# Kernel tuning notes

Measured on AMD Instinct MI355X. Metric: run time of the kernel, lower is better.

Reference implementation:

```python
import jax, jax.numpy as jnp
import numpy as np

D_MODEL = 512
N_HEADS = 8
D_KV = 64
EPS = 1e-6
ROPE_THETA = 10000.0


def _rms_norm(x, w):
    # T5-style RMSNorm: no mean subtraction, no bias, variance in fp32.
    var = jnp.mean(x.astype(jnp.float32) ** 2, axis=-1, keepdims=True)
    return (x * jax.lax.rsqrt(var + EPS)).astype(x.dtype) * w


def _rope_cos_sin(pos, dk):
    # pos: [B, T] int -> cos/sin: [B, 1, T, dk]
    inv_freq = 1.0 / (ROPE_THETA ** (jnp.arange(0, dk, 2, dtype=jnp.float32) / dk))
    ang = pos.astype(jnp.float32)[:, :, None] * inv_freq[None, None, :]  # [B,T,dk/2]
    ang = jnp.concatenate([ang, ang], axis=-1)                            # [B,T,dk]
    return jnp.cos(ang)[:, None], jnp.sin(ang)[:, None]


def _rotate_half(x):
    h = x.shape[-1] // 2
    return jnp.concatenate([-x[..., h:], x[..., :h]], axis=-1)


def _mha(x, mask, wq, wk, wv, wo, pos=None):
    # x: [B, T, D]; mask: [B, H, T, T] additive
    B, T, _ = x.shape
    def proj(w):
        return (x @ w).reshape(B, T, N_HEADS, D_KV).transpose(0, 2, 1, 3)  # [B,H,T,dk]
    q, k, v = proj(wq), proj(wk), proj(wv)
    if pos is not None:
        cos, sin = _rope_cos_sin(pos, D_KV)
        cos, sin = cos.astype(x.dtype), sin.astype(x.dtype)
        q = q * cos + _rotate_half(q) * sin
        k = k * cos + _rotate_half(k) * sin
    scale = 1.0 / np.sqrt(D_KV)
    scores = jnp.einsum('bhqd,bhkd->bhqk', q, k) * scale + mask
    attn = jax.nn.softmax(scores.astype(jnp.float32), axis=-1).astype(scores.dtype)
    out = jnp.einsum('bhqk,bhkd->bhqd', attn, v)
    out = out.transpose(0, 2, 1, 3).reshape(B, T, N_HEADS * D_KV)
    return out @ wo


def setup_inputs() -> dict:
    key = jax.random.key(0)
    ks = jax.random.split(key, 12)
    B, T = 8, 1024
    s = 1.0 / np.sqrt(D_MODEL)
    inp = {
        'h': jax.random.normal(ks[0], (B, T, D_MODEL), dtype=jnp.float32),
        'pos': jnp.broadcast_to(jnp.arange(T, dtype=jnp.int64 if jax.config.jax_enable_x64 else jnp.int32)[None, :], (B, T)),
        't_mask': jnp.zeros((B, N_HEADS, T, T), dtype=jnp.float32),
        'g_mask': jnp.zeros((T, N_HEADS, B, B), dtype=jnp.float32),
        'ln_t_w': jnp.ones((D_MODEL,), dtype=jnp.float32),
        'ln_g_w': jnp.ones((D_MODEL,), dtype=jnp.float32),
    }
    names = ['wq_t', 'wk_t', 'wv_t', 'wo_t', 'wq_g', 'wk_g', 'wv_g', 'wo_g']
    for i, n in enumerate(names):
        inp[n] = jax.random.normal(ks[i + 1], (D_MODEL, D_MODEL), dtype=jnp.float32) * s
    return inp


def reference(h, pos, t_mask, g_mask, ln_t_w, ln_g_w,
              wq_t, wk_t, wv_t, wo_t, wq_g, wk_g, wv_g, wo_g):
    # --- time attention (over T axis, with RoPE) ---
    normed = _rms_norm(h, ln_t_w)
    attn_t = _mha(normed, t_mask, wq_t, wk_t, wv_t, wo_t, pos=pos)
    h = h + attn_t  # dropout p=0 (eval)
    # --- group attention (over B axis, no RoPE) ---
    h = h.transpose(1, 0, 2)  # [T, B, D]
    normed = _rms_norm(h, ln_g_w)
    attn_g = _mha(normed, g_mask, wq_g, wk_g, wv_g, wo_g, pos=None)
    h = h + attn_g
    return h.transpose(1, 0, 2)  # back to [B, T, D]
```

## Files before the change

### kernel.cpp

```cpp
#include <hip/hip_runtime.h>
#include <hip/hip_bf16.h>
#include <math.h>


typedef __bf16 bf16x8 __attribute__((ext_vector_type(8)));
typedef __bf16 bf16x4 __attribute__((ext_vector_type(4)));
typedef float  f32x4  __attribute__((ext_vector_type(4)));

#define LN1E4_OVER_32 0.2878231366242558f

__device__ __forceinline__ void gld16(const void* g, void* l) {
    __builtin_amdgcn_global_load_lds((const __attribute__((address_space(1))) void*)g,
                                     (__attribute__((address_space(3))) void*)l,
                                     16, 0, 0);
}

__global__ __launch_bounds__(256) void transpose_w(
    const float* w0, const float* w1, const float* w2, const float* w3,
    const float* w4, const float* w5, const float* w6, const float* w7,
    __bf16* qkvT_t, __bf16* oT_t, __bf16* qkvT_g, __bf16* oT_g)
{
    int mat = blockIdx.z;
    const float* src; __bf16* dst; int rowOff;
    switch (mat) {
        case 0: src=w0; dst=qkvT_t; rowOff=0;    break;
        case 1: src=w1; dst=qkvT_t; rowOff=512;  break;
        case 2: src=w2; dst=qkvT_t; rowOff=1024; break;
        case 3: src=w3; dst=oT_t;   rowOff=0;    break;
        case 4: src=w4; dst=qkvT_g; rowOff=0;    break;
        case 5: src=w5; dst=qkvT_g; rowOff=512;  break;
        case 6: src=w6; dst=qkvT_g; rowOff=1024; break;
        default: src=w7; dst=oT_g;  rowOff=0;    break;
    }
    __shared__ float tile[32][33];
    int n0 = blockIdx.x * 32, k0 = blockIdx.y * 32;
    int tt = threadIdx.x;
    int kr = tt >> 3, nc = (tt & 7) * 4;
    float4 v = *(const float4*)(src + (size_t)(k0 + kr) * 512 + n0 + nc);
    tile[kr][nc+0] = v.x; tile[kr][nc+1] = v.y; tile[kr][nc+2] = v.z; tile[kr][nc+3] = v.w;
    __syncthreads();
    int nr = tt >> 3, kc = (tt & 7) * 4;
    bf16x4 o;
    o[0] = (__bf16)tile[kc+0][nr]; o[1] = (__bf16)tile[kc+1][nr];
    o[2] = (__bf16)tile[kc+2][nr]; o[3] = (__bf16)tile[kc+3][nr];
    *(bf16x4*)(dst + (size_t)(rowOff + n0 + nr) * 512 + k0 + kc) = o;
}

__global__ __launch_bounds__(256) void rmsnorm_k(
    const float* __restrict__ x, const float* __restrict__ w,
    __bf16* __restrict__ y, int remap)
{
    int row = blockIdx.x * 4 + (threadIdx.x >> 6);
    int l = threadIdx.x & 63;
    const float* xr = x + (size_t)row * 512 + l * 8;
    float4 a = *(const float4*)xr;
    float4 b = *(const float4*)(xr + 4);
    float ss = a.x*a.x + a.y*a.y + a.z*a.z + a.w*a.w
             + b.x*b.x + b.y*b.y + b.z*b.z + b.w*b.w;
    for (int m = 1; m < 64; m <<= 1) ss += __shfl_xor(ss, m);
    float rms = rsqrtf(ss * (1.0f / 512.0f) + 1e-6f);
    float4 wa = *(const float4*)(w + l * 8);
    float4 wb = *(const float4*)(w + l * 8 + 4);
    int orow = remap ? ((row & 1023) * 8 + (row >> 10)) : row;
    bf16x8 o;
    o[0] = (__bf16)(a.x * rms * wa.x); o[1] = (__bf16)(a.y * rms * wa.y);
    o[2] = (__bf16)(a.z * rms * wa.z); o[3] = (__bf16)(a.w * rms * wa.w);
    o[4] = (__bf16)(b.x * rms * wb.x); o[5] = (__bf16)(b.y * rms * wb.y);
    o[6] = (__bf16)(b.z * rms * wb.z); o[7] = (__bf16)(b.w * rms * wb.w);
    *(bf16x8*)(y + (size_t)orow * 512 + l * 8) = o;
}

__global__ __launch_bounds__(256) void gemm_ep(
    const __bf16* __restrict__ A, const __bf16* __restrict__ Bt,
    const int* __restrict__ pos, const float* __restrict__ resid,
    float* __restrict__ outF,
    __bf16* __restrict__ o0, __bf16* __restrict__ o1, __bf16* __restrict__ o2,
    int mode)
{
    __shared__ float fsm[4][1088];
    __bf16* As = (__bf16*)fsm;
    __bf16* Bs = As + 4096;
    int tid = threadIdx.x;
    int l = tid & 63, w = tid >> 6;
    int l16 = l & 15, quad = l >> 4;
    int wm = w >> 1, wn = w & 1;
    int mblk = blockIdx.y * 128, nblk = blockIdx.x * 128;
    f32x4 acc[4][4] = {};

    for (int k0 = 0; k0 < 512; k0 += 32) {
        __syncthreads();
        #pragma unroll
        for (int i = 0; i < 2; ++i) {
            int idx = i * 256 + tid;
            int row = idx >> 2, c8 = (idx & 3) * 8;
            gld16(A  + (size_t)(mblk + row) * 512 + k0 + c8, (char*)As + (size_t)idx * 16);
            gld16(Bt + (size_t)(nblk + row) * 512 + k0 + c8, (char*)Bs + (size_t)idx * 16);
        }
        __syncthreads();
        bf16x8 aF[4], bF[4];
        #pragma unroll
        for (int mt = 0; mt < 4; mt++) aF[mt] = *(bf16x8*)(As + (wm * 64 + mt * 16 + l16) * 32 + quad * 8);
        #pragma unroll
        for (int nt = 0; nt < 4; nt++) bF[nt] = *(bf16x8*)(Bs + (wn * 64 + nt * 16 + l16) * 32 + quad * 8);
        #pragma unroll
        for (int mt = 0; mt < 4; mt++)
            #pragma unroll
            for (int nt = 0; nt < 4; nt++)
                acc[mt][nt] = __builtin_amdgcn_mfma_f32_16x16x32_bf16(aF[mt], bF[nt], acc[mt][nt], 0, 0, 0);
    }
    __syncthreads();

    int colbase = nblk + wn * 64;
    __bf16* bw = ((__bf16*)fsm) + w * 1536;
    float*  fw = (float*)((char*)fsm + w * 4352);
    int rbrow = l >> 3, rbch = (l & 7) * 8;

    if (mode == 0 || mode == 2) {
        int mat = colbase >> 9;
        int hh  = (colbase & 511) >> 6;
        __bf16* dst = (mat == 0) ? o0 : (mat == 1) ? o1 : o2;
        bool isQ = (mat == 0), isV = (mat == 2);
        if (mode == 0 && !isV) {
            float f0 = __expf((float)l16        * -LN1E4_OVER_32);
            float f1 = __expf((float)(16 + l16) * -LN1E4_OVER_32);
            #pragma unroll
            for (int mt = 0; mt < 4; mt++) {
                int grow0 = mblk + wm * 64 + mt * 16;
                int b = grow0 >> 10, t0 = grow0 & 1023;
                int4 p4 = *(const int4*)&pos[grow0 + quad * 4];
                const int pa[4] = {p4.x, p4.y, p4.z, p4.w};
                #pragma unroll
                for (int r = 0; r < 4; r++) {
                    float p = (float)pa[r];
                    #pragma unroll
                    for (int nt = 0; nt < 2; nt++) {
                        int i = nt * 16 + l16;
                        float ang = p * (nt ? f1 : f0);
                        float c, s; __sincosf(ang, &s, &c);
                        float x1 = acc[mt][nt][r], x2 = acc[mt][nt + 2][r];
                        float y1 = x1 * c - x2 * s;
                        float y2 = x2 * c + x1 * s;
                        if (isQ) { y1 *= 0.125f; y2 *= 0.125f; }
                        bw[(quad * 4 + r) * 72 + i]      = (__bf16)y1;
                        bw[(quad * 4 + r) * 72 + i + 32] = (__bf16)y2;
                    }
                }
                #pragma unroll
                for (int i = 0; i < 2; ++i) {
                    int rr = rbrow + i * 8;
                    bf16x8 vv = *(bf16x8*)&bw[rr * 72 + rbch];
                    *(bf16x8*)&dst[((size_t)(b * 8 + hh) * 1024 + t0 + rr) * 64 + rbch] = vv;
                }
            }
        } else if (mode == 0) {
            #pragma unroll
            for (int mt = 0; mt < 4; mt++) {
                #pragma unroll
                for (int nt = 0; nt < 4; nt++)
                    #pragma unroll
                    for (int r = 0; r < 4; r++)
                        bw[(nt * 16 + l16) * 24 + quad * 4 + r] = (__bf16)acc[mt][nt][r];
                int grow0 = mblk + wm * 64 + mt * 16;
                int b = grow0 >> 10, t0 = grow0 & 1023;
                #pragma unroll
                for (int i = 0; i < 2; ++i) {
                    int li = i * 64 + l;
                    int d = li >> 1, t8 = (li & 1) * 8;
                    bf16x8 vv = *(bf16x8*)&bw[d * 24 + t8];
                    *(bf16x8*)&dst[((size_t)(b * 8 + hh) * 64 + d) * 1024 + t0 + t8] = vv;
                }
            }
        } else {
            #pragma unroll
            for (int mt = 0; mt < 4; mt++) {
                int grow0 = mblk + wm * 64 + mt * 16;
                #pragma unroll
                for (int nt = 0; nt < 4; nt++)
                    #pragma unroll
                    for (int r = 0; r < 4; r++) {
                        float v = acc[mt][nt][r];
                        if (isQ) v *= 0.125f;
                        bw[(quad * 4 + r) * 72 + nt * 16 + l16] = (__bf16)v;
                    }
                #pragma unroll
                for (int i = 0; i < 2; ++i) {
                    int rr = rbrow + i * 8;
                    int grow = grow0 + rr;
                    int t = grow >> 3, bq = grow & 7;
                    bf16x8 vv = *(bf16x8*)&bw[rr * 72 + rbch];
                    *(bf16x8*)&dst[(((size_t)t * 8 + hh) * 8 + bq) * 64 + rbch] = vv;
                }
            }
        }
    } else {
        #pragma unroll
        for (int mt = 0; mt < 4; mt++) {
            int grow0 = mblk + wm * 64 + mt * 16;
            #pragma unroll
            for (int nt = 0; nt < 4; nt++)
                #pragma unroll
                for (int r = 0; r < 4; r++)
                    fw[(quad * 4 + r) * 68 + nt * 16 + l16] = acc[mt][nt][r];
            #pragma unroll
            for (int i = 0; i < 4; ++i) {
                int rr = i * 4 + (l >> 4);
                int c4 = (l & 15) * 4;
                f32x4 a4 = *(f32x4*)&fw[rr * 68 + c4];
                int grow = grow0 + rr;
                int orow = (mode == 3) ? (((grow & 7) << 10) + (grow >> 3)) : grow;
                size_t oi = (size_t)orow * 512 + colbase + c4;
                f32x4 r4 = *(const f32x4*)&resid[oi];
                r4 += a4;
                *(f32x4*)&outF[oi] = r4;
            }
        }
    }
}

__global__ __launch_bounds__(256) void flash_t(
    const __bf16* __restrict__ q, const __bf16* __restrict__ k,
    const __bf16* __restrict__ vt, const float* __restrict__ tmask,
    __bf16* __restrict__ ctx)
{
    int bh = blockIdx.y;
    int w = threadIdx.x >> 6, l = threadIdx.x & 63;
    int l16 = l & 15, quad = l >> 4;
    int qb0 = blockIdx.x * 64;
    int q0 = qb0 + w * 16;

    __shared__ __bf16 Ks[64 * 72];
    __shared__ __bf16 Vs[64 * 72];
    __shared__ __bf16 Ps[4][16 * 72];
    __shared__ float  Ms[64 * 64];

    bf16x8 aQ0, aQ1;
    {
        const __bf16* qp = q + ((size_t)bh * 1024 + q0 + l16) * 64 + quad * 8;
        aQ0 = *(const bf16x8*)qp;
        aQ1 = *(const bf16x8*)(qp + 32);
    }
    f32x4 o[4] = {};
    float m_i[4], l_i[4];
    #pragma unroll
    for (int r = 0; r < 4; r++) { m_i[r] = -INFINITY; l_i[r] = 0.0f; }

    const float* mbase = tmask + (size_t)bh * 1024 * 1024;

    for (int jb = 0; jb < 1024; jb += 64) {
        __syncthreads();
        #pragma unroll
        for (int it = 0; it < 2; ++it) {
            int c = threadIdx.x + it * 256;
            int row = c >> 3, col = (c & 7) << 3;
            *(bf16x8*)&Ks[row * 72 + col] = *(const bf16x8*)&k [((size_t)bh * 1024 + jb + row) * 64 + col];
            *(bf16x8*)&Vs[row * 72 + col] = *(const bf16x8*)&vt[((size_t)bh * 64 + row) * 1024 + jb + col];
        }
        #pragma unroll
        for (int it = 0; it < 4; ++it) {
            int c = it * 256 + threadIdx.x;
            int row = c >> 4, ch = c & 15;
            gld16(mbase + (size_t)(qb0 + row) * 1024 + jb + ch * 4, (char*)Ms + (size_t)c * 16);
        }
        __syncthreads();

        f32x4 s[4] = {};
        #pragma unroll
        for (int nt = 0; nt < 4; nt++) {
            bf16x8 b0 = *(bf16x8*)&Ks[(nt * 16 + l16) * 72 + quad * 8];
            bf16x8 b1 = *(bf16x8*)&Ks[(nt * 16 + l16) * 72 + 32 + quad * 8];
            s[nt] = __builtin_amdgcn_mfma_f32_16x16x32_bf16(aQ0, b0, s[nt], 0, 0, 0);
            s[nt] = __builtin_amdgcn_mfma_f32_16x16x32_bf16(aQ1, b1, s[nt], 0, 0, 0);
        }
        #pragma unroll
        for (int r = 0; r < 4; r++)
            #pragma unroll
            for (int nt = 0; nt < 4; nt++)
                s[nt][r] += Ms[(w * 16 + quad * 4 + r) * 64 + nt * 16 + l16];

        float alpha[4];
        #pragma unroll
        for (int r = 0; r < 4; r++) {
            float mx = fmaxf(fmaxf(s[0][r], s[1][r]), fmaxf(s[2][r], s[3][r]));
            mx = fmaxf(mx, __shfl_xor(mx, 1));
            mx = fmaxf(mx, __shfl_xor(mx, 2));
            mx = fmaxf(mx, __shfl_xor(mx, 4));
            mx = fmaxf(mx, __shfl_xor(mx, 8));
            float mn = fmaxf(m_i[r], mx);
            alpha[r] = __expf(m_i[r] - mn);
            m_i[r] = mn;
            float rs = 0.0f;
            #pragma unroll
            for (int nt = 0; nt < 4; nt++) {
                float p = __expf(s[nt][r] - mn);
                s[nt][r] = p;
                rs += p;
            }
            rs += __shfl_xor(rs, 1);
            rs += __shfl_xor(rs, 2);
            rs += __shfl_xor(rs, 4);
            rs += __shfl_xor(rs, 8);
            l_i[r] = l_i[r] * alpha[r] + rs;
        }
        #pragma unroll
        for (int dt = 0; dt < 4; dt++)
            #pragma unroll
            for (int r = 0; r < 4; r++) o[dt][r] *= alpha[r];

        __bf16* ps = Ps[w];
        #pragma unroll
        for (int nt = 0; nt < 4; nt++)
            #pragma unroll
            for (int r = 0; r < 4; r++)
                ps[(quad * 4 + r) * 72 + nt * 16 + l16] = (__bf16)s[nt][r];
        bf16x8 aP0 = *(bf16x8*)&ps[l16 * 72 + quad * 8];
        bf16x8 aP1 = *(bf16x8*)&ps[l16 * 72 + 32 + quad * 8];
        #pragma unroll
        for (int dt = 0; dt < 4; dt++) {
            bf16x8 bv0 = *(bf16x8*)&Vs[(dt * 16 + l16) * 72 + quad * 8];
            bf16x8 bv1 = *(bf16x8*)&Vs[(dt * 16 + l16) * 72 + 32 + quad * 8];
            o[dt] = __builtin_amdgcn_mfma_f32_16x16x32_bf16(aP0, bv0, o[dt], 0, 0, 0);
            o[dt] = __builtin_amdgcn_mfma_f32_16x16x32_bf16(aP1, bv1, o[dt], 0, 0, 0);
        }
    }

    int b = bh >> 3, h = bh & 7;
    __bf16* ps = Ps[w];
    #pragma unroll
    for (int dt = 0; dt < 4; dt++)
        #pragma unroll
        for (int r = 0; r < 4; r++)
            ps[(quad * 4 + r) * 72 + dt * 16 + l16] = (__bf16)(o[dt][r] / l_i[r]);
    int rbrow = l >> 3, rbch = (l & 7) * 8;
    #pragma unroll
    for (int i = 0; i < 2; ++i) {
        int rr = rbrow + i * 8;
        bf16x8 vv = *(bf16x8*)&ps[rr * 72 + rbch];
        *(bf16x8*)&ctx[((size_t)b * 1024 + q0 + rr) * 512 + h * 64 + rbch] = vv;
    }
}

__global__ __launch_bounds__(256) void group_attn(
    const __bf16* __restrict__ qg, const __bf16* __restrict__ kg,
    const __bf16* __restrict__ vg, const float* __restrict__ gmask,
    __bf16* __restrict__ ctxg)
{
    int tid = blockIdx.x * 256 + threadIdx.x;
    int t = tid >> 6, h = (tid >> 3) & 7, bq = tid & 7;
    size_t base = ((size_t)t * 8 + h) * 512;

    float qv[64];
    #pragma unroll
    for (int d0 = 0; d0 < 64; d0 += 8) {
        bf16x8 qq = *(const bf16x8*)&qg[base + (size_t)bq * 64 + d0];
        #pragma unroll
        for (int u = 0; u < 8; u++) qv[d0 + u] = (float)qq[u];
    }
    float s[8];
    #pragma unroll
    for (int j = 0; j < 8; j++) {
        float acc = 0.0f;
        #pragma unroll
        for (int d0 = 0; d0 < 64; d0 += 8) {
            bf16x8 kk = *(const bf16x8*)&kg[base + (size_t)j * 64 + d0];
            #pragma unroll
            for (int u = 0; u < 8; u++) acc += qv[d0 + u] * (float)kk[u];
        }
        s[j] = acc + gmask[(((size_t)t * 8 + h) * 8 + bq) * 8 + j];
    }
    float mx = s[0];
    #pragma unroll
    for (int j = 1; j < 8; j++) mx = fmaxf(mx, s[j]);
    float sum = 0.0f;
    #pragma unroll
    for (int j = 0; j < 8; j++) { s[j] = __expf(s[j] - mx); sum += s[j]; }
    float inv = 1.0f / sum;

    #pragma unroll
    for (int d0 = 0; d0 < 64; d0 += 8) {
        float o8[8] = {};
        #pragma unroll
        for (int j = 0; j < 8; j++) {
            bf16x8 vv = *(const bf16x8*)&vg[base + (size_t)j * 64 + d0];
            float pj = s[j];
            #pragma unroll
            for (int u = 0; u < 8; u++) o8[u] += pj * (float)vv[u];
        }
        bf16x8 ob;
        #pragma unroll
        for (int u = 0; u < 8; u++) ob[u] = (__bf16)(o8[u] * inv);
        *(bf16x8*)&ctxg[((size_t)t * 8 + bq) * 512 + h * 64 + d0] = ob;
    }
}

extern "C" void kernel_launch(void* const* d_in, const int* in_sizes, int n_in,
                              void* d_out, int out_size, void* d_ws, size_t ws_size,
                              hipStream_t stream)
{
    const float* h      = (const float*)d_in[0];
    const int*   pos    = (const int*)  d_in[1];
    const float* t_mask = (const float*)d_in[2];
    const float* g_mask = (const float*)d_in[3];
    const float* ln_t_w = (const float*)d_in[4];
    const float* ln_g_w = (const float*)d_in[5];
    const float* wq_t = (const float*)d_in[6];
    const float* wk_t = (const float*)d_in[7];
    const float* wv_t = (const float*)d_in[8];
    const float* wo_t = (const float*)d_in[9];
    const float* wq_g = (const float*)d_in[10];
    const float* wk_g = (const float*)d_in[11];
    const float* wv_g = (const float*)d_in[12];
    const float* wo_g = (const float*)d_in[13];
    float* out = (float*)d_out;

    char* ws = (char*)d_ws;
    const size_t MB = 1ull << 20;
    __bf16* qkvT_t = (__bf16*)ws;
    __bf16* oT_t   = qkvT_t + 786432;
    __bf16* qkvT_g = qkvT_t + 1048576;
    __bf16* oT_g   = qkvT_t + 1835008;
    __bf16* normed = (__bf16*)(ws + 4 * MB);
    __bf16* qb     = (__bf16*)(ws + 12 * MB);
    __bf16* kb     = (__bf16*)(ws + 20 * MB);
    __bf16* vb     = (__bf16*)(ws + 28 * MB);
    __bf16* ctx    = (__bf16*)(ws + 36 * MB);
    float*  h2     = (float*) (ws + 44 * MB);

    transpose_w<<<dim3(16, 16, 8), 256, 0, stream>>>(
        wq_t, wk_t, wv_t, wo_t, wq_g, wk_g, wv_g, wo_g,
        qkvT_t, oT_t, qkvT_g, oT_g);

    rmsnorm_k<<<2048, 256, 0, stream>>>(h, ln_t_w, normed, 0);
    gemm_ep<<<dim3(12, 64), 256, 0, stream>>>(normed, qkvT_t, pos, nullptr, nullptr,
                                              qb, kb, vb, 0);
    flash_t<<<dim3(16, 64), 256, 0, stream>>>(qb, kb, vb, t_mask, ctx);
    gemm_ep<<<dim3(4, 64), 256, 0, stream>>>(ctx, oT_t, nullptr, h, h2,
                                             nullptr, nullptr, nullptr, 1);

    rmsnorm_k<<<2048, 256, 0, stream>>>(h2, ln_g_w, normed, 1);
    gemm_ep<<<dim3(12, 64), 256, 0, stream>>>(normed, qkvT_g, nullptr, nullptr, nullptr,
                                              qb, kb, vb, 2);
    group_attn<<<256, 256, 0, stream>>>(qb, kb, vb, g_mask, ctx);
    gemm_ep<<<dim3(4, 64), 256, 0, stream>>>(ctx, oT_g, nullptr, h2, out,
                                             nullptr, nullptr, nullptr, 3);
}
```

Measured before the change: 569.8 us.

## Split output GEMM into 64-row kernel and prefetch mask into registers

Adds a dedicated gemm_o kernel with 64x128 tiles for the output projections plus residual add. It doubles the grid from 256 to 512 blocks to improve CU occupancy on the small N=512 GEMMs. The QKV gemm_ep kernel loses its residual path and now uses 16KB of shared memory instead of about 17KB. Flash attention drops its shared-memory mask staging and instead loads each thread's mask elements directly into registers with nontemporal loads, prefetching the next block, which trades LDS traffic and a sync for more register pressure.

```diff
diff --git a/kernel.cpp b/kernel.cpp
--- a/kernel.cpp
+++ b/kernel.cpp
@@ -72,14 +72,13 @@
 
 __global__ __launch_bounds__(256) void gemm_ep(
     const __bf16* __restrict__ A, const __bf16* __restrict__ Bt,
-    const int* __restrict__ pos, const float* __restrict__ resid,
-    float* __restrict__ outF,
+    const int* __restrict__ pos,
     __bf16* __restrict__ o0, __bf16* __restrict__ o1, __bf16* __restrict__ o2,
     int mode)
 {
-    __shared__ float fsm[4][1088];
-    __bf16* As = (__bf16*)fsm;
-    __bf16* Bs = As + 4096;
+    __shared__ __bf16 smem[8192];
+    __bf16* As = smem;
+    __bf16* Bs = smem + 4096;
     int tid = threadIdx.x;
     int l = tid & 63, w = tid >> 6;
     int l16 = l & 15, quad = l >> 4;
@@ -111,108 +110,142 @@
     __syncthreads();
 
     int colbase = nblk + wn * 64;
-    __bf16* bw = ((__bf16*)fsm) + w * 1536;
-    float*  fw = (float*)((char*)fsm + w * 4352);
+    __bf16* bw = smem + w * 1536;
     int rbrow = l >> 3, rbch = (l & 7) * 8;
 
-    if (mode == 0 || mode == 2) {
-        int mat = colbase >> 9;
-        int hh  = (colbase & 511) >> 6;
-        __bf16* dst = (mat == 0) ? o0 : (mat == 1) ? o1 : o2;
-        bool isQ = (mat == 0), isV = (mat == 2);
-        if (mode == 0 && !isV) {
-            float f0 = __expf((float)l16        * -LN1E4_OVER_32);
-            float f1 = __expf((float)(16 + l16) * -LN1E4_OVER_32);
-            #pragma unroll
-            for (int mt = 0; mt < 4; mt++) {
-                int grow0 = mblk + wm * 64 + mt * 16;
-                int b = grow0 >> 10, t0 = grow0 & 1023;
-                int4 p4 = *(const int4*)&pos[grow0 + quad * 4];
-                const int pa[4] = {p4.x, p4.y, p4.z, p4.w};
+    int mat = colbase >> 9;
+    int hh  = (colbase & 511) >> 6;
+    __bf16* dst = (mat == 0) ? o0 : (mat == 1) ? o1 : o2;
+    bool isQ = (mat == 0), isV = (mat == 2);
+    if (mode == 0 && !isV) {
+        float f0 = __expf((float)l16        * -LN1E4_OVER_32);
+        float f1 = __expf((float)(16 + l16) * -LN1E4_OVER_32);
+        #pragma unroll
+        for (int mt = 0; mt < 4; mt++) {
+            int grow0 = mblk + wm * 64 + mt * 16;
+            int b = grow0 >> 10, t0 = grow0 & 1023;
+            int4 p4 = *(const int4*)&pos[grow0 + quad * 4];
+            const int pa[4] = {p4.x, p4.y, p4.z, p4.w};
+            #pragma unroll
+            for (int r = 0; r < 4; r++) {
+                float p = (float)pa[r];
                 #pragma unroll
-                for (int r = 0; r < 4; r++) {
-                    float p = (float)pa[r];
-                    #pragma unroll
-                    for (int nt = 0; nt < 2; nt++) {
-                        int i = nt * 16 + l16;
-                        float ang = p * (nt ? f1 : f0);
-                        float c, s; __sincosf(ang, &s, &c);
-                        float x1 = acc[mt][nt][r], x2 = acc[mt][nt + 2][r];
-                        float y1 = x1 * c - x2 * s;
-                        float y2 = x2 * c + x1 * s;
-                        if (isQ) { y1 *= 0.125f; y2 *= 0.125f; }
-                        bw[(quad * 4 + r) * 72 + i]      = (__bf16)y1;
-                        bw[(quad * 4 + r) * 72 + i + 32] = (__bf16)y2;
-                    }
-                }
-                #pragma unroll
-                for (int i = 0; i < 2; ++i) {
-                    int rr = rbrow + i * 8;
-                    bf16x8 vv = *(bf16x8*)&bw[rr * 72 + rbch];
-                    *(bf16x8*)&dst[((size_t)(b * 8 + hh) * 1024 + t0 + rr) * 64 + rbch] = vv;
+                for (int nt = 0; nt < 2; nt++) {
+                    int i = nt * 16 + l16;
+                    float ang = p * (nt ? f1 : f0);
+                    float c, s; __sincosf(ang, &s, &c);
+                    float x1 = acc[mt][nt][r], x2 = acc[mt][nt + 2][r];
+                    float y1 = x1 * c - x2 * s;
+                    float y2 = x2 * c + x1 * s;
+                    if (isQ) { y1 *= 0.125f; y2 *= 0.125f; }
+                    bw[(quad * 4 + r) * 72 + i]      = (__bf16)y1;
+                    bw[(quad * 4 + r) * 72 + i + 32] = (__bf16)y2;
                 }
             }
-        } else if (mode == 0) {
-            #pragma unroll
-            for (int mt = 0; mt < 4; mt++) {
-                #pragma unroll
-                for (int nt = 0; nt < 4; nt++)
-                    #pragma unroll
-                    for (int r = 0; r < 4; r++)
-                        bw[(nt * 16 + l16) * 24 + quad * 4 + r] = (__bf16)acc[mt][nt][r];
-                int grow0 = mblk + wm * 64 + mt * 16;
-                int b = grow0 >> 10, t0 = grow0 & 1023;
-                #pragma unroll
-                for (int i = 0; i < 2; ++i) {
-                    int li = i * 64 + l;
-                    int d = li >> 1, t8 = (li & 1) * 8;
-                    bf16x8 vv = *(bf16x8*)&bw[d * 24 + t8];
-                    *(bf16x8*)&dst[((size_t)(b * 8 + hh) * 64 + d) * 1024 + t0 + t8] = vv;
-                }
+            #pragma unroll
+            for (int i = 0; i < 2; ++i) {
+                int rr = rbrow + i * 8;
+                bf16x8 vv = *(bf16x8*)&bw[rr * 72 + rbch];
+                *(bf16x8*)&dst[((size_t)(b * 8 + hh) * 1024 + t0 + rr) * 64 + rbch] = vv;
             }
-        } else {
-            #pragma unroll
-            for (int mt = 0; mt < 4; mt++) {
-                int grow0 = mblk + wm * 64 + mt * 16;
-                #pragma unroll
-                for (int nt = 0; nt < 4; nt++)
-                    #pragma unroll
-                    for (int r = 0; r < 4; r++) {
-                        float v = acc[mt][nt][r];
-                        if (isQ) v *= 0.125f;
-                        bw[(quad * 4 + r) * 72 + nt * 16 + l16] = (__bf16)v;
-                    }
-                #pragma unroll
-                for (int i = 0; i < 2; ++i) {
-                    int rr = rbrow + i * 8;
-                    int grow = grow0 + rr;
-                    int t = grow >> 3, bq = grow & 7;
-                    bf16x8 vv = *(bf16x8*)&bw[rr * 72 + rbch];
-                    *(bf16x8*)&dst[(((size_t)t * 8 + hh) * 8 + bq) * 64 + rbch] = vv;
-                }
-            }
-        }
-    } else {
+        }
+    } else if (mode == 0) {
         #pragma unroll
         for (int mt = 0; mt < 4; mt++) {
-            int grow0 = mblk + wm * 64 + mt * 16;
             #pragma unroll
             for (int nt = 0; nt < 4; nt++)
                 #pragma unroll
                 for (int r = 0; r < 4; r++)
-                    fw[(quad * 4 + r) * 68 + nt * 16 + l16] = acc[mt][nt][r];
-            #pragma unroll
-            for (int i = 0; i < 4; ++i) {
-                int rr = i * 4 + (l >> 4);
-                int c4 = (l & 15) * 4;
-                f32x4 a4 = *(f32x4*)&fw[rr * 68 + c4];
+                    bw[(nt * 16 + l16) * 24 + quad * 4 + r] = (__bf16)acc[mt][nt][r];
+            int grow0 = mblk + wm * 64 + mt * 16;
+            int b = grow0 >> 10, t0 = grow0 & 1023;
+            #pragma unroll
+            for (int i = 0; i < 2; ++i) {
+                int li = i * 64 + l;
+                int d = li >> 1, t8 = (li & 1) * 8;
+                bf16x8 vv = *(bf16x8*)&bw[d * 24 + t8];
+                *(bf16x8*)&dst[((size_t)(b * 8 + hh) * 64 + d) * 1024 + t0 + t8] = vv;
+            }
+        }
+    } else {
+        #pragma unroll
+        for (int mt = 0; mt < 4; mt++) {
+            int grow0 = mblk + wm * 64 + mt * 16;
+            #pragma unroll
+            for (int nt = 0; nt < 4; nt++)
+                #pragma unroll
+                for (int r = 0; r < 4; r++) {
+                    float v = acc[mt][nt][r];
+                    if (isQ) v *= 0.125f;
+                    bw[(quad * 4 + r) * 72 + nt * 16 + l16] = (__bf16)v;
+                }
+            #pragma unroll
+            for (int i = 0; i < 2; ++i) {
+                int rr = rbrow + i * 8;
                 int grow = grow0 + rr;
-                int orow = (mode == 3) ? (((grow & 7) << 10) + (grow >> 3)) : grow;
-                size_t oi = (size_t)orow * 512 + colbase + c4;
-                f32x4 r4 = *(const f32x4*)&resid[oi];
-                r4 += a4;
-                *(f32x4*)&outF[oi] = r4;
+                int t = grow >> 3, bq = grow & 7;
+                bf16x8 vv = *(bf16x8*)&bw[rr * 72 + rbch];
+                *(bf16x8*)&dst[(((size_t)t * 8 + hh) * 8 + bq) * 64 + rbch] = vv;
             }
+        }
+    }
+}
+
+__global__ __launch_bounds__(256) void gemm_o(
+    const __bf16* __restrict__ A, const __bf16* __restrict__ Bt,
+    const float* __restrict__ resid, float* __restrict__ outF, int remap)
+{
+    __shared__ float fsm[4][1088];
+    __bf16* As = (__bf16*)fsm;
+    __bf16* Bs = As + 2048;
+    int tid = threadIdx.x;
+    int l = tid & 63, w = tid >> 6;
+    int l16 = l & 15, quad = l >> 4;
+    int mblk = blockIdx.y * 64, nblk = blockIdx.x * 128;
+    f32x4 acc[8] = {};
+
+    for (int k0 = 0; k0 < 512; k0 += 32) {
+        __syncthreads();
+        {
+            int row = tid >> 2, c8 = (tid & 3) * 8;
+            gld16(A + (size_t)(mblk + row) * 512 + k0 + c8, (char*)As + (size_t)tid * 16);
+        }
+        #pragma unroll
+        for (int i = 0; i < 2; ++i) {
+            int idx = i * 256 + tid;
+            int row = idx >> 2, c8 = (idx & 3) * 8;
+            gld16(Bt + (size_t)(nblk + row) * 512 + k0 + c8, (char*)Bs + (size_t)idx * 16);
+        }
+        __syncthreads();
+        bf16x8 aF = *(bf16x8*)(As + (w * 16 + l16) * 32 + quad * 8);
+        #pragma unroll
+        for (int nt = 0; nt < 8; nt++) {
+            bf16x8 bF = *(bf16x8*)(Bs + (nt * 16 + l16) * 32 + quad * 8);
+            acc[nt] = __builtin_amdgcn_mfma_f32_16x16x32_bf16(aF, bF, acc[nt], 0, 0, 0);
+        }
+    }
+    __syncthreads();
+
+    float* fw = (float*)((char*)fsm + w * 4352);
+    int grow0 = mblk + w * 16;
+    #pragma unroll
+    for (int nh = 0; nh < 2; nh++) {
+        #pragma unroll
+        for (int nt = 0; nt < 4; nt++)
+            #pragma unroll
+            for (int r = 0; r < 4; r++)
+                fw[(quad * 4 + r) * 68 + nt * 16 + l16] = acc[nh * 4 + nt][r];
+        #pragma unroll
+        for (int i = 0; i < 4; ++i) {
+            int rr = i * 4 + (l >> 4);
+            int c4 = (l & 15) * 4;
+            f32x4 a4 = *(f32x4*)&fw[rr * 68 + c4];
+            int grow = grow0 + rr;
+            int orow = remap ? (((grow & 7) << 10) + (grow >> 3)) : grow;
+            size_t oi = (size_t)orow * 512 + nblk + nh * 64 + c4;
+            f32x4 r4 = *(const f32x4*)&resid[oi];
+            r4 += a4;
+            *(f32x4*)&outF[oi] = r4;
         }
     }
 }
@@ -225,13 +258,11 @@
     int bh = blockIdx.y;
     int w = threadIdx.x >> 6, l = threadIdx.x & 63;
     int l16 = l & 15, quad = l >> 4;
-    int qb0 = blockIdx.x * 64;
-    int q0 = qb0 + w * 16;
+    int q0 = blockIdx.x * 64 + w * 16;
 
     __shared__ __bf16 Ks[64 * 72];
     __shared__ __bf16 Vs[64 * 72];
     __shared__ __bf16 Ps[4][16 * 72];
-    __shared__ float  Ms[64 * 64];
 
     bf16x8 aQ0, aQ1;
     {
@@ -244,7 +275,13 @@
     #pragma unroll
     for (int r = 0; r < 4; r++) { m_i[r] = -INFINITY; l_i[r] = 0.0f; }
 
-    const float* mbase = tmask + (size_t)bh * 1024 * 1024;
+    const float* mrow = tmask + (size_t)bh * 1024 * 1024 + (size_t)(q0 + quad * 4) * 1024 + l16;
+    float mc[16];
+    #pragma unroll
+    for (int r = 0; r < 4; r++)
+        #pragma unroll
+        for (int nt = 0; nt < 4; nt++)
+            mc[r * 4 + nt] = __builtin_nontemporal_load(mrow + (size_t)r * 1024 + nt * 16);
 
     for (int jb = 0; jb < 1024; jb += 64) {
         __syncthreads();
@@ -255,13 +292,18 @@
             *(bf16x8*)&Ks[row * 72 + col] = *(const bf16x8*)&k [((size_t)bh * 1024 + jb + row) * 64 + col];
             *(bf16x8*)&Vs[row * 72 + col] = *(const bf16x8*)&vt[((size_t)bh * 64 + row) * 1024 + jb + col];
         }
-        #pragma unroll
-        for (int it = 0; it < 4; ++it) {
-            int c = it * 256 + threadIdx.x;
-            int row = c >> 4, ch = c & 15;
-            gld16(mbase + (size_t)(qb0 + row) * 1024 + jb + ch * 4, (char*)Ms + (size_t)c * 16);
-        }
-        __syncthreads();
+        __syncthreads();
+
+        float mn_[16];
+        {
+            int jb2 = (jb + 64) & 1023;
+            const float* mr2 = mrow + jb2;
+            #pragma unroll
+            for (int r = 0; r < 4; r++)
+                #pragma unroll
+                for (int nt = 0; nt < 4; nt++)
+                    mn_[r * 4 + nt] = __builtin_nontemporal_load(mr2 + (size_t)r * 1024 + nt * 16);
+        }
 
         f32x4 s[4] = {};
         #pragma unroll
@@ -275,7 +317,7 @@
         for (int r = 0; r < 4; r++)
             #pragma unroll
             for (int nt = 0; nt < 4; nt++)
-                s[nt][r] += Ms[(w * 16 + quad * 4 + r) * 64 + nt * 16 + l16];
+                s[nt][r] += mc[r * 4 + nt];
 
         float alpha[4];
         #pragma unroll
@@ -321,6 +363,9 @@
             o[dt] = __builtin_amdgcn_mfma_f32_16x16x32_bf16(aP0, bv0, o[dt], 0, 0, 0);
             o[dt] = __builtin_amdgcn_mfma_f32_16x16x32_bf16(aP1, bv1, o[dt], 0, 0, 0);
         }
+
+        #pragma unroll
+        for (int i = 0; i < 16; i++) mc[i] = mn_[i];
     }
 
     int b = bh >> 3, h = bh & 7;
@@ -430,16 +475,12 @@
         qkvT_t, oT_t, qkvT_g, oT_g);
 
     rmsnorm_k<<<2048, 256, 0, stream>>>(h, ln_t_w, normed, 0);
-    gemm_ep<<<dim3(12, 64), 256, 0, stream>>>(normed, qkvT_t, pos, nullptr, nullptr,
-                                              qb, kb, vb, 0);
+    gemm_ep<<<dim3(12, 64), 256, 0, stream>>>(normed, qkvT_t, pos, qb, kb, vb, 0);
     flash_t<<<dim3(16, 64), 256, 0, stream>>>(qb, kb, vb, t_mask, ctx);
-    gemm_ep<<<dim3(4, 64), 256, 0, stream>>>(ctx, oT_t, nullptr, h, h2,
-                                             nullptr, nullptr, nullptr, 1);
+    gemm_o<<<dim3(4, 128), 256, 0, stream>>>(ctx, oT_t, h, h2, 0);
 
     rmsnorm_k<<<2048, 256, 0, stream>>>(h2, ln_g_w, normed, 1);
-    gemm_ep<<<dim3(12, 64), 256, 0, stream>>>(normed, qkvT_g, nullptr, nullptr, nullptr,
-                                              qb, kb, vb, 2);
+    gemm_ep<<<dim3(12, 64), 256, 0, stream>>>(normed, qkvT_g, nullptr, qb, kb, vb, 2);
     group_attn<<<256, 256, 0, stream>>>(qb, kb, vb, g_mask, ctx);
-    gemm_ep<<<dim3(4, 64), 256, 0, stream>>>(ctx, oT_g, nullptr, h2, out,
-                                             nullptr, nullptr, nullptr, 3);
-}
+    gemm_o<<<dim3(4, 128), 256, 0, stream>>>(ctx, oT_g, h2, out, 1);
+}
```

New measurement: 520.1 us. 8.7% less time.
